# Kernel tuning notes

Hardware: AMD Instinct MI355X
Metric: run time of the kernel (lower is better)

The kernel has to match this reference:

```python
import jax, jax.numpy as jnp
import numpy as np

SEQ_LEN, BATCH, HIDDEN, OUT = 512, 4096, 2048, 10


def setup_inputs() -> dict:
    key = jax.random.key(0)
    ks = jax.random.split(key, 7)
    return {
        "x": jax.random.normal(ks[0], (SEQ_LEN, BATCH), jnp.float32),
        "Wx": jax.random.normal(ks[1], (HIDDEN, 1), jnp.float32) * 0.05,
        "bx": jax.random.normal(ks[2], (HIDDEN,), jnp.float32) * 0.05,
        "Wh": jax.random.normal(ks[3], (1, HIDDEN), jnp.float32) * 0.05,
        "bh": jax.random.normal(ks[4], (1,), jnp.float32) * 0.05,
        "Wy": jax.random.normal(ks[5], (OUT, HIDDEN), jnp.float32) * 0.05,
        "by": jax.random.normal(ks[6], (OUT,), jnp.float32) * 0.05,
    }


def reference(x, Wx, bx, Wh, bh, Wy, by):
    # x: [T, B]; input_dim == 1 structurally (torch code reshapes x[i] to (B, 1)).
    B = x.shape[1]
    H = Wx.shape[0]
    wx = Wx[:, 0]  # [H]

    def step(h, xt):
        # linear_x(x_t): (B,1) @ (1,H) -> outer product, [B, H]
        x_out = xt[:, None] * wx[None, :] + bx
        # linear_h(h): [B, H] @ [H, 1] -> [B, 1], broadcasts into the add (as in torch)
        h_out = h @ Wh.T + bh
        h_new = jnp.tanh(x_out + h_out)
        return h_new, None

    h0 = jnp.zeros((B, H), x.dtype)
    h_final, _ = jax.lax.scan(step, h0, x)
    logits = h_final @ Wy.T + by  # [B, OUT]
    return jax.nn.softmax(logits, axis=-1)
```

## Files before the change

kernel.cpp:

```cpp
#include <hip/hip_runtime.h>
#include <math.h>


#define SEQ   512
#define BATCH 4096
#define HID   2048
#define NOUT  10
#define KPL   32
#define NS    560
#define ROWQ  9

#define S_LOc   (-10.0f)
#define S_H     (20.0f / 559.0f)
#define S_INVH  (559.0f / 20.0f)
#define S_BIAS  (10.0f * S_INVH)
#define NSM1F   559.0f
#define NSM4F   556.0f
#define U_SCALE (8.0f / 14.0f)
#define U_BIAS  4.0f
#define UCMAXF  7.99951f

#define TABLE_FLOATS (NS * ROWQ * 4)
#define WSA_FLOATS (4096 + 14 * 4096)
#define WSB_FLOATS (4096 + 4 * 4096)
#define DZ14 43.0f
#define DZ9  69.875f

__device__ __forceinline__ float fast_exp2(float v) { return __builtin_amdgcn_exp2f(v); }
__device__ __forceinline__ float fast_rcp(float v)  { return __builtin_amdgcn_rcpf(v); }
__device__ __forceinline__ float med3(float a, float lo, float hi) {
    return __builtin_amdgcn_fmed3f(a, lo, hi);
}
__device__ __forceinline__ float fast_tanh(float a) {
    const float C = 2.8853900817779268f;
    return __builtin_fmaf(-2.0f, fast_rcp(fast_exp2(C * a) + 1.0f), 1.0f);
}
__device__ __forceinline__ float wave_sum(float v) {
#pragma unroll
    for (int m = 1; m < 64; m <<= 1) v += __shfl_xor(v, m, 64);
    return v;
}
__device__ __forceinline__ float combine_eval(float z255, int nn, float dz,
                                              const float* baseA, const float* baseB,
                                              int split, int b) {
    float p = z255 / dz;
    int   c = min(max((int)floorf(p) - 1, 0), nn - 4);
    float t = p - (float)c;
    float a0 = t, a1 = t - 1.0f, a2 = t - 2.0f, a3 = t - 3.0f;
    float m01 = a0 * a1, m23 = a2 * a3;
    float w0 = a1 * m23 * (-1.0f / 6.0f), w1 = a0 * m23 * 0.5f;
    float w2 = m01 * a3 * (-0.5f),        w3 = m01 * a2 * (1.0f / 6.0f);
    float y[4];
#pragma unroll
    for (int i = 0; i < 4; ++i) {
        int n = c + i;
        const float* ptr = (n < split) ? (baseA + (size_t)n * 4096)
                                       : (baseB + (size_t)(n - split) * 4096);
        y[i] = ptr[b];
    }
    return __builtin_fmaf(w0, y[0], w1 * y[1]) + __builtin_fmaf(w2, y[2], w3 * y[3]);
}

__global__ __launch_bounds__(256) void k_coef(const float* __restrict__ Wx, const float* __restrict__ bx,
                                              const float* __restrict__ Wh, const float* __restrict__ bh,
                                              float* __restrict__ tab_g) {
    __shared__ float red[256];
    __shared__ float Gn[32];
    const int k    = blockIdx.x;
    const int node = threadIdx.x & 31;
    const int jc   = threadIdx.x >> 5;
    const int cell = node >> 2, nn = node & 3;
    const float sn = S_LOc + (float)k * S_H;
    const float xi_n = (nn == 0) ? 0.923879533f : (nn == 1) ? 0.382683432f
                     : (nn == 2) ? -0.382683432f : -0.923879533f;
    const float un = (-7.0f + ((float)cell + 0.5f) * 1.75f) + 0.875f * xi_n;
    float p = 0.0f;
    const int j0 = jc * 256;
#pragma unroll 4
    for (int j = j0; j < j0 + 256; ++j)
        p += Wh[j] * fast_tanh(__builtin_fmaf(Wx[j], un, bx[j] + sn));
    red[threadIdx.x] = p;
    __syncthreads();
    if (threadIdx.x < 32) {
        float V = bh[0];
#pragma unroll
        for (int c = 0; c < 8; ++c) V += red[threadIdx.x + 32 * c];
        Gn[threadIdx.x] = __builtin_fmaf(V, S_INVH, S_BIAS);
    }
    __syncthreads();
    float4* wq = (float4*)tab_g;
    if (threadIdx.x < 8) {
        const int c = threadIdx.x;
        float G0 = Gn[4*c+0], G1 = Gn[4*c+1], G2 = Gn[4*c+2], G3 = Gn[4*c+3];
        float d03 = G0 - G3, d12 = G1 - G2;
        float a0 = 0.25f * (G0 + G1 + G2 + G3);
        float a1 = 0.5f * (0.923879533f * d03 + 0.382683432f * d12);
        float a2 = 0.5f * 0.707106781f * (G0 - G1 - G2 + G3);
        float a3 = 0.5f * (0.382683432f * d03 - 0.923879533f * d12);
        wq[k * ROWQ + c] = make_float4(a0 - a2, a1 - 3.0f * a3, 2.0f * a2, 4.0f * a3);
    } else if (threadIdx.x == 8) {
        wq[k * ROWQ + 8] = make_float4(0.f, 0.f, 0.f, 0.f);
    }
}

__global__ __launch_bounds__(256) void k_scan_seg(const float* __restrict__ x,
                                                  const float* __restrict__ bh,
                                                  const float* __restrict__ tab_g,
                                                  float* __restrict__ z255,
                                                  float* __restrict__ baseA,
                                                  float* __restrict__ baseB,
                                                  int split, float dz) {
    __shared__ float4 tabs[5200];
    {
        const float4* src = (const float4*)tab_g;
        for (int i = threadIdx.x; i < NS * ROWQ; i += 256) tabs[i] = src[i];
    }
    __syncthreads();
    const int blk = blockIdx.x;
    const int seg  = (blk < 16) ? 0 : 1;
    const int node = seg ? (blk - 16) >> 4 : 0;
    const int eb   = seg ? (blk - 16) & 15 : blk;
    const int b    = eb * 256 + threadIdx.x;

    const int t0     = seg ? 255 : 0;
    const int nsteps = seg ? 256 : 255;

    float zm1 = seg ? __builtin_fmaf((float)node, dz, -1.0f)
                    : med3(__builtin_fmaf(bh[0], S_INVH, S_BIAS), 0.0f, NSM1F) - 1.0f;

    auto step1 = [&](float xi, float xi2, int ci) {
        float kf  = med3(zm1, 0.0f, NSM4F);
        int   kzi = (int)kf;
        int   idx = ((kzi << 3) + kzi) + ci;
        float4 q0 = tabs[idx];
        float4 q1 = tabs[idx + ROWQ];
        float4 q2 = tabs[idx + 2 * ROWQ];
        float4 q3 = tabs[idx + 3 * ROWQ];
        float kzf = (float)kzi;
        float zc2 = med3(zm1, -1.0f, 558.0f);
        float e   = zc2 - kzf;
        float c0 = e + 1.0f, c1 = e, c2 = e - 1.0f, c3 = e - 2.0f;
        float n01 = c0 * c1, n23 = c2 * c3;
        float ws0 = c1 * n23 * (-1.0f / 6.0f), ws1 = c0 * n23 * 0.5f;
        float ws2 = n01 * c3 * (-0.5f),        ws3 = n01 * c2 * (1.0f / 6.0f);
        float l0 = __builtin_fmaf(q0.y, xi, q0.x), h0 = __builtin_fmaf(q0.w, xi, q0.z);
        float l1 = __builtin_fmaf(q1.y, xi, q1.x), h1 = __builtin_fmaf(q1.w, xi, q1.z);
        float l2 = __builtin_fmaf(q2.y, xi, q2.x), h2 = __builtin_fmaf(q2.w, xi, q2.z);
        float l3 = __builtin_fmaf(q3.y, xi, q3.x), h3 = __builtin_fmaf(q3.w, xi, q3.z);
        float r0 = __builtin_fmaf(h0, xi2, l0);
        float r1 = __builtin_fmaf(h1, xi2, l1);
        float r2 = __builtin_fmaf(h2, xi2, l2);
        float r3 = __builtin_fmaf(h3, xi2, l3);
        float A  = __builtin_fmaf(ws0, r0, ws1 * r1);
        float B  = __builtin_fmaf(ws2, r2, __builtin_fmaf(ws3, r3, -1.0f));
        zm1 = A + B;
    };

    float cur[8], nxt[8];
#pragma unroll
    for (int i = 0; i < 8; ++i)
        cur[i] = x[(size_t)min(t0 + i, SEQ - 1) * BATCH + b];

    const int full = nsteps >> 3, tail = nsteps & 7;
    for (int c = 0; c < full; ++c) {
        const int nb = t0 + (c + 1) * 8;
#pragma unroll
        for (int i = 0; i < 8; ++i)
            nxt[i] = x[(size_t)min(nb + i, SEQ - 1) * BATCH + b];
        float xiA[8], xi2A[8]; int ciA[8];
#pragma unroll
        for (int i = 0; i < 8; ++i) {
            float uc = med3(__builtin_fmaf(cur[i], U_SCALE, U_BIAS), 0.0f, UCMAXF);
            int   ci = (int)uc;
            float xi = __builtin_fmaf(2.0f, uc - (float)ci, -1.0f);
            xiA[i] = xi; xi2A[i] = xi * xi; ciA[i] = ci;
        }
#pragma unroll
        for (int i = 0; i < 8; ++i) step1(xiA[i], xi2A[i], ciA[i]);
#pragma unroll
        for (int i = 0; i < 8; ++i) cur[i] = nxt[i];
    }
    for (int i = 0; i < tail; ++i) {
        float uc = med3(__builtin_fmaf(cur[i], U_SCALE, U_BIAS), 0.0f, UCMAXF);
        int   ci = (int)uc;
        float xi = __builtin_fmaf(2.0f, uc - (float)ci, -1.0f);
        step1(xi, xi * xi, ci);
    }

    const float z = zm1 + 1.0f;
    if (seg == 0) z255[b] = z;
    else {
        float* p = (node < split) ? (baseA + (size_t)node * 4096)
                                  : (baseB + (size_t)(node - split) * 4096);
        p[b] = z;
    }
}

__global__ __launch_bounds__(256) void k_combine(const float* __restrict__ baseA,
                                                 const float* __restrict__ baseB,
                                                 int split, int nn, float dz,
                                                 float* __restrict__ zs) {
    const int b = blockIdx.x * 256 + threadIdx.x;
    float zz = combine_eval(zs[b], nn, dz, baseA, baseB, split, b);
    zs[b] = __builtin_fmaf(zz, S_H, S_LOc);
}

__global__ __launch_bounds__(256) void head_combine_A(
    const float* __restrict__ x,  const float* __restrict__ Wx,
    const float* __restrict__ bx, const float* __restrict__ Wy,
    const float* __restrict__ by, const float* __restrict__ ws,
    float* __restrict__ out)
{
    const int lane = threadIdx.x & 63;
    const int wave = threadIdx.x >> 6;
    const int b    = blockIdx.x * 4 + wave;

    float zz = combine_eval(ws[b], 14, DZ14, ws + 4096, ws + 4096, 14, b);
    const float s = __builtin_fmaf(zz, S_H, S_LOc);

    const float C  = 2.8853900817779268f;
    const float u  = x[(size_t)(SEQ - 1) * BATCH + b];
    const float sc = s * C;
    float acc[NOUT];
#pragma unroll
    for (int i = 0; i < NOUT; ++i) acc[i] = 0.0f;
#pragma unroll 4
    for (int k = 0; k < KPL; ++k) {
        const int j = k * 64 + lane;
        float arg = __builtin_fmaf(u, Wx[j] * C, bx[j] * C) + sc;
        float r   = fast_rcp(fast_exp2(arg) + 1.0f);
        float th  = __builtin_fmaf(-2.0f, r, 1.0f);
#pragma unroll
        for (int i = 0; i < NOUT; ++i)
            acc[i] = __builtin_fmaf(Wy[i * HID + j], th, acc[i]);
    }
#pragma unroll
    for (int i = 0; i < NOUT; ++i) acc[i] = wave_sum(acc[i]) + by[i];
    float m = acc[0];
#pragma unroll
    for (int i = 1; i < NOUT; ++i) m = fmaxf(m, acc[i]);
    const float L2E = 1.4426950408889634f;
    float ev[NOUT]; float Z = 0.0f;
#pragma unroll
    for (int i = 0; i < NOUT; ++i) { ev[i] = fast_exp2((acc[i] - m) * L2E); Z += ev[i]; }
    const float rz = fast_rcp(Z);
    if (lane == 0) {
#pragma unroll
        for (int i = 0; i < NOUT; ++i) out[(size_t)b * NOUT + i] = ev[i] * rz;
    }
}

__global__ __launch_bounds__(256) void rnn_scan_exact(
    const float* __restrict__ x,  const float* __restrict__ Wx,
    const float* __restrict__ bx, const float* __restrict__ Wh,
    const float* __restrict__ bh, float* __restrict__ s_out)
{
    const int lane = threadIdx.x & 63;
    const int wave = threadIdx.x >> 6;
    const int b    = blockIdx.x * 4 + wave;
    const float C = 2.8853900817779268f;
    float wxs[KPL], bxs[KPL], whn[KPL];
    float swh = 0.0f;
#pragma unroll
    for (int k = 0; k < KPL; ++k) {
        const int j = k * 64 + lane;
        const float w = Wh[j];
        wxs[k] = Wx[j] * C; bxs[k] = bx[j] * C; whn[k] = -2.0f * w; swh += w;
    }
    swh = wave_sum(swh);
    const float bh0 = bh[0];
    const float K0  = bh0 + swh;
    float s = bh0, u = x[b];
    for (int t = 0; t < SEQ - 1; ++t) {
        float u_next = x[(size_t)(t + 1) * BATCH + b];
        const float sc = s * C;
        float p = 0.0f;
#pragma unroll
        for (int k = 0; k < KPL; ++k) {
            float arg = __builtin_fmaf(u, wxs[k], bxs[k]) + sc;
            float r   = fast_rcp(fast_exp2(arg) + 1.0f);
            p = __builtin_fmaf(whn[k], r, p);
        }
        s = K0 + wave_sum(p);
        u = u_next;
    }
    if (lane == 0) s_out[b] = s;
}

__global__ __launch_bounds__(256) void rnn_head_exact(
    const float* __restrict__ x,  const float* __restrict__ Wx,
    const float* __restrict__ bx, const float* __restrict__ Wy,
    const float* __restrict__ by, const float* __restrict__ s_in,
    float* __restrict__ out)
{
    const int lane = threadIdx.x & 63;
    const int wave = threadIdx.x >> 6;
    const int b    = blockIdx.x * 4 + wave;
    const float C  = 2.8853900817779268f;
    const float s  = s_in[b];
    const float u  = x[(size_t)(SEQ - 1) * BATCH + b];
    const float sc = s * C;
    float acc[NOUT];
#pragma unroll
    for (int i = 0; i < NOUT; ++i) acc[i] = 0.0f;
#pragma unroll 4
    for (int k = 0; k < KPL; ++k) {
        const int j = k * 64 + lane;
        float arg = __builtin_fmaf(u, Wx[j] * C, bx[j] * C) + sc;
        float r   = fast_rcp(fast_exp2(arg) + 1.0f);
        float th  = __builtin_fmaf(-2.0f, r, 1.0f);
#pragma unroll
        for (int i = 0; i < NOUT; ++i)
            acc[i] = __builtin_fmaf(Wy[i * HID + j], th, acc[i]);
    }
#pragma unroll
    for (int i = 0; i < NOUT; ++i) acc[i] = wave_sum(acc[i]) + by[i];
    float m = acc[0];
#pragma unroll
    for (int i = 1; i < NOUT; ++i) m = fmaxf(m, acc[i]);
    const float L2E = 1.4426950408889634f;
    float ev[NOUT]; float Z = 0.0f;
#pragma unroll
    for (int i = 0; i < NOUT; ++i) { ev[i] = fast_exp2((acc[i] - m) * L2E); Z += ev[i]; }
    const float rz = fast_rcp(Z);
    if (lane == 0) {
#pragma unroll
        for (int i = 0; i < NOUT; ++i) out[(size_t)b * NOUT + i] = ev[i] * rz;
    }
}

extern "C" void kernel_launch(void* const* d_in, const int* in_sizes, int n_in,
                              void* d_out, int out_size, void* d_ws, size_t ws_size,
                              hipStream_t stream)
{
    const float* x  = (const float*)d_in[0];
    const float* Wx = (const float*)d_in[1];
    const float* bx = (const float*)d_in[2];
    const float* Wh = (const float*)d_in[3];
    const float* bh = (const float*)d_in[4];
    const float* Wy = (const float*)d_in[5];
    const float* by = (const float*)d_in[6];
    float* out = (float*)d_out;
    float* wf  = (float*)d_ws;

    if (ws_size >= (size_t)WSA_FLOATS * sizeof(float)) {
        k_coef<<<NS, 256, 0, stream>>>(Wx, bx, Wh, bh, out);
        k_scan_seg<<<16 + 14 * 16, 256, 0, stream>>>(x, bh, out, wf,
                                                     wf + 4096, wf + 4096, 14, DZ14);
        head_combine_A<<<BATCH / 4, 256, 0, stream>>>(x, Wx, bx, Wy, by, wf, out);
    } else if (ws_size >= (size_t)WSB_FLOATS * sizeof(float)) {
        k_coef<<<NS, 256, 0, stream>>>(Wx, bx, Wh, bh, out);
        k_scan_seg<<<16 + 9 * 16, 256, 0, stream>>>(x, bh, out, wf,
                                                    out + TABLE_FLOATS, wf + 4096, 5, DZ9);
        k_combine<<<16, 256, 0, stream>>>(out + TABLE_FLOATS, wf + 4096, 5, 9, DZ9, wf);
        rnn_head_exact<<<BATCH / 4, 256, 0, stream>>>(x, Wx, bx, Wy, by, wf, out);
    } else {
        rnn_scan_exact<<<BATCH / 4, 256, 0, stream>>>(x, Wx, bx, Wh, bh, wf);
        rnn_head_exact<<<BATCH / 4, 256, 0, stream>>>(x, Wx, bx, Wy, by, wf, out);
    }
}
```

Measured before the change: 141.0 us.

## Speculate table index with linear interpolation to shorten serial scan dependency chain

The per-step table lookup in the sequential scan now takes its row index from a cheaply computed linear-interpolation estimate (zf), while the accurate cubic-Lagrange value (za) is computed alongside and resynchronized every 8 steps. The aim is to take the LDS load latency and cubic weight computation off the loop-carried critical path. Index arithmetic also moves to byte offsets with the -1 bias folded into the table pointer. The risk is that wrong rows get selected when the linear estimate drifts from the cubic one, which changes numerical results.

```diff
diff --git a/kernel.cpp b/kernel.cpp
--- a/kernel.cpp
+++ b/kernel.cpp
@@ -15,7 +15,6 @@
 #define S_INVH  (559.0f / 20.0f)
 #define S_BIAS  (10.0f * S_INVH)
 #define NSM1F   559.0f
-#define NSM4F   556.0f
 #define U_SCALE (8.0f / 14.0f)
 #define U_BIAS  4.0f
 #define UCMAXF  7.99951f
@@ -116,6 +115,7 @@
         for (int i = threadIdx.x; i < NS * ROWQ; i += 256) tabs[i] = src[i];
     }
     __syncthreads();
+    const char* tabc = (const char*)tabs;
     const int blk = blockIdx.x;
     const int seg  = (blk < 16) ? 0 : 1;
     const int node = seg ? (blk - 16) >> 4 : 0;
@@ -125,20 +125,47 @@
     const int t0     = seg ? 255 : 0;
     const int nsteps = seg ? 256 : 255;
 
-    float zm1 = seg ? __builtin_fmaf((float)node, dz, -1.0f)
-                    : med3(__builtin_fmaf(bh[0], S_INVH, S_BIAS), 0.0f, NSM1F) - 1.0f;
-
-    auto step1 = [&](float xi, float xi2, int ci) {
-        float kf  = med3(zm1, 0.0f, NSM4F);
-        int   kzi = (int)kf;
-        int   idx = ((kzi << 3) + kzi) + ci;
-        float4 q0 = tabs[idx];
-        float4 q1 = tabs[idx + ROWQ];
-        float4 q2 = tabs[idx + 2 * ROWQ];
-        float4 q3 = tabs[idx + 3 * ROWQ];
-        float kzf = (float)kzi;
-        float zc2 = med3(zm1, -1.0f, 558.0f);
-        float e   = zc2 - kzf;
+    float za = seg ? (float)node * dz
+                   : med3(__builtin_fmaf(bh[0], S_INVH, S_BIAS), 0.0f, NSM1F);
+    float zf = za;
+
+    auto stepF = [&](float xi, float xi2, int cib) {
+        float m  = med3(zf, 1.0f, 557.0f);
+        int   km = (int)m;
+        const float4* qp = (const float4*)(tabc + (km * 144 + cib));
+        float4 q1 = qp[ROWQ];
+        float4 q2 = qp[2 * ROWQ];
+        float4 q0 = qp[0];
+        float4 q3 = qp[3 * ROWQ];
+        float kmf = (float)km;
+        float tf  = zf - kmf;
+        float e   = med3(za, 0.0f, NSM1F) - kmf;
+        float c0 = e + 1.0f, c1 = e, c2 = e - 1.0f, c3 = e - 2.0f;
+        float n01 = c0 * c1, n23 = c2 * c3;
+        float ws0 = c1 * n23 * (-1.0f / 6.0f), ws1 = c0 * n23 * 0.5f;
+        float ws2 = n01 * c3 * (-0.5f),        ws3 = n01 * c2 * (1.0f / 6.0f);
+        float l1 = __builtin_fmaf(q1.y, xi, q1.x), h1 = __builtin_fmaf(q1.w, xi, q1.z);
+        float l2 = __builtin_fmaf(q2.y, xi, q2.x), h2 = __builtin_fmaf(q2.w, xi, q2.z);
+        float r1 = __builtin_fmaf(h1, xi2, l1);
+        float r2 = __builtin_fmaf(h2, xi2, l2);
+        zf = __builtin_fmaf(tf, r2 - r1, r1);
+        float l0 = __builtin_fmaf(q0.y, xi, q0.x), h0 = __builtin_fmaf(q0.w, xi, q0.z);
+        float l3 = __builtin_fmaf(q3.y, xi, q3.x), h3 = __builtin_fmaf(q3.w, xi, q3.z);
+        float r0 = __builtin_fmaf(h0, xi2, l0);
+        float r3 = __builtin_fmaf(h3, xi2, l3);
+        za = __builtin_fmaf(ws0, r0, ws1 * r1) + __builtin_fmaf(ws2, r2, ws3 * r3);
+    };
+
+    auto stepA = [&](float xi, float xi2, int cib) {
+        float m  = med3(za, 1.0f, 557.0f);
+        int   km = (int)m;
+        const float4* qp = (const float4*)(tabc + (km * 144 + cib));
+        float4 q0 = qp[0];
+        float4 q1 = qp[ROWQ];
+        float4 q2 = qp[2 * ROWQ];
+        float4 q3 = qp[3 * ROWQ];
+        float kmf = (float)km;
+        float e   = med3(za, 0.0f, NSM1F) - kmf;
         float c0 = e + 1.0f, c1 = e, c2 = e - 1.0f, c3 = e - 2.0f;
         float n01 = c0 * c1, n23 = c2 * c3;
         float ws0 = c1 * n23 * (-1.0f / 6.0f), ws1 = c0 * n23 * 0.5f;
@@ -151,9 +178,7 @@
         float r1 = __builtin_fmaf(h1, xi2, l1);
         float r2 = __builtin_fmaf(h2, xi2, l2);
         float r3 = __builtin_fmaf(h3, xi2, l3);
-        float A  = __builtin_fmaf(ws0, r0, ws1 * r1);
-        float B  = __builtin_fmaf(ws2, r2, __builtin_fmaf(ws3, r3, -1.0f));
-        zm1 = A + B;
+        za = __builtin_fmaf(ws0, r0, ws1 * r1) + __builtin_fmaf(ws2, r2, ws3 * r3);
     };
 
     float cur[8], nxt[8];
@@ -167,16 +192,17 @@
 #pragma unroll
         for (int i = 0; i < 8; ++i)
             nxt[i] = x[(size_t)min(nb + i, SEQ - 1) * BATCH + b];
-        float xiA[8], xi2A[8]; int ciA[8];
+        float xiA[8], xi2A[8]; int cibA[8];
 #pragma unroll
         for (int i = 0; i < 8; ++i) {
             float uc = med3(__builtin_fmaf(cur[i], U_SCALE, U_BIAS), 0.0f, UCMAXF);
             int   ci = (int)uc;
             float xi = __builtin_fmaf(2.0f, uc - (float)ci, -1.0f);
-            xiA[i] = xi; xi2A[i] = xi * xi; ciA[i] = ci;
+            xiA[i] = xi; xi2A[i] = xi * xi; cibA[i] = (ci << 4) - 144;
         }
 #pragma unroll
-        for (int i = 0; i < 8; ++i) step1(xiA[i], xi2A[i], ciA[i]);
+        for (int i = 0; i < 8; ++i) stepF(xiA[i], xi2A[i], cibA[i]);
+        zf = za;
 #pragma unroll
         for (int i = 0; i < 8; ++i) cur[i] = nxt[i];
     }
@@ -184,10 +210,10 @@
         float uc = med3(__builtin_fmaf(cur[i], U_SCALE, U_BIAS), 0.0f, UCMAXF);
         int   ci = (int)uc;
         float xi = __builtin_fmaf(2.0f, uc - (float)ci, -1.0f);
-        step1(xi, xi * xi, ci);
-    }
-
-    const float z = zm1 + 1.0f;
+        stepA(xi, xi * xi, (ci << 4) - 144);
+    }
+
+    const float z = za;
     if (seg == 0) z255[b] = z;
     else {
         float* p = (node < split) ? (baseA + (size_t)node * 4096)
```

Result: no change. 141.7 us (+0.6%).

## Split scan step into fast linear predictor and deferred cubic correction with manual LDS pipelining

Applied to the files above, without the earlier changes.

Restructures the serial recurrence step so that the critical path only depends on a cheap linear interpolation between the two middle table rows (zf). The full cubic Lagrange evaluation (za) is computed one step later, overlapped with the next step's LDS reads. Hand-written ds_read_b128 with explicit waitcnts and sched barriers control the latency hiding. This shortens the per-step dependency chain, but the index now comes from an approximate z, which risks accuracy drift. It also depends on inline asm and a raw LDS address cast.

```diff
diff --git a/kernel.cpp b/kernel.cpp
--- a/kernel.cpp
+++ b/kernel.cpp
@@ -15,7 +15,6 @@
 #define S_INVH  (559.0f / 20.0f)
 #define S_BIAS  (10.0f * S_INVH)
 #define NSM1F   559.0f
-#define NSM4F   556.0f
 #define U_SCALE (8.0f / 14.0f)
 #define U_BIAS  4.0f
 #define UCMAXF  7.99951f
@@ -25,6 +24,8 @@
 #define WSB_FLOATS (4096 + 4 * 4096)
 #define DZ14 43.0f
 #define DZ9  69.875f
+
+typedef float f32x4 __attribute__((ext_vector_type(4)));
 
 __device__ __forceinline__ float fast_exp2(float v) { return __builtin_amdgcn_exp2f(v); }
 __device__ __forceinline__ float fast_rcp(float v)  { return __builtin_amdgcn_rcpf(v); }
@@ -103,6 +104,51 @@
     }
 }
 
+
+#define STEP_BODY(xi_, xi2_, cib_, FIRST)                                      \
+{                                                                              \
+    float m_   = med3(zf, 1.0f, 557.0f);                                       \
+    int   km_  = (int)m_;                                                      \
+    float kmf_ = (float)km_;                                                   \
+    float tf_  = med3(zf - kmf_, -1.0f, 2.0f);                                 \
+    int   ab_  = km_ * 144 + (cib_);                                           \
+    f32x4 q0_, q1_, q2_, q3_;                                                  \
+    asm volatile("ds_read_b128 %0, %4 offset:144\n\t"                          \
+                 "ds_read_b128 %1, %4 offset:288\n\t"                          \
+                 "ds_read_b128 %2, %4 offset:0\n\t"                            \
+                 "ds_read_b128 %3, %4 offset:432"                              \
+                 : "=v"(q1_), "=v"(q2_), "=v"(q0_), "=v"(q3_)                  \
+                 : "v"(ab_) : "memory");                                       \
+    if (!(FIRST)) {                                                            \
+        asm volatile("s_waitcnt lgkmcnt(4)" ::: "memory");                     \
+        __builtin_amdgcn_sched_barrier(0);                                     \
+        float e_  = med3(za, 0.0f, NSM1F) - kmfp;                              \
+        float c0_ = e_ + 1.0f, c1_ = e_, c2_ = e_ - 1.0f, c3_ = e_ - 2.0f;     \
+        float n01_ = c0_ * c1_, n23_ = c2_ * c3_;                              \
+        float w0_ = c1_ * n23_ * (-1.0f / 6.0f), w1_ = c0_ * n23_ * 0.5f;      \
+        float w2_ = n01_ * c3_ * (-0.5f),        w3_ = n01_ * c2_ * (1.0f/6.0f);\
+        float l0_ = __builtin_fmaf(p0[1], xip, p0[0]);                         \
+        float h0_ = __builtin_fmaf(p0[3], xip, p0[2]);                         \
+        float l3_ = __builtin_fmaf(p3[1], xip, p3[0]);                         \
+        float h3_ = __builtin_fmaf(p3[3], xip, p3[2]);                         \
+        float r0_ = __builtin_fmaf(h0_, xi2p, l0_);                            \
+        float r3_ = __builtin_fmaf(h3_, xi2p, l3_);                            \
+        za = __builtin_fmaf(w0_, r0_, w1_ * r1p)                               \
+           + __builtin_fmaf(w2_, r2p, w3_ * r3_);                              \
+    }                                                                          \
+    asm volatile("s_waitcnt lgkmcnt(2)" ::: "memory");                         \
+    __builtin_amdgcn_sched_barrier(0);                                         \
+    float l1_ = __builtin_fmaf(q1_[1], (xi_), q1_[0]);                         \
+    float h1_ = __builtin_fmaf(q1_[3], (xi_), q1_[2]);                         \
+    float l2_ = __builtin_fmaf(q2_[1], (xi_), q2_[0]);                         \
+    float h2_ = __builtin_fmaf(q2_[3], (xi_), q2_[2]);                         \
+    float r1_ = __builtin_fmaf(h1_, (xi2_), l1_);                              \
+    float r2_ = __builtin_fmaf(h2_, (xi2_), l2_);                              \
+    zf = __builtin_fmaf(tf_, r2_ - r1_, r1_);                                  \
+    p0 = q0_; p3 = q3_;                                                        \
+    xip = (xi_); xi2p = (xi2_); kmfp = kmf_; r1p = r1_; r2p = r2_;             \
+}
+
 __global__ __launch_bounds__(256) void k_scan_seg(const float* __restrict__ x,
                                                   const float* __restrict__ bh,
                                                   const float* __restrict__ tab_g,
@@ -116,6 +162,7 @@
         for (int i = threadIdx.x; i < NS * ROWQ; i += 256) tabs[i] = src[i];
     }
     __syncthreads();
+    const int tb = (int)(size_t)(&tabs[0]);
     const int blk = blockIdx.x;
     const int seg  = (blk < 16) ? 0 : 1;
     const int node = seg ? (blk - 16) >> 4 : 0;
@@ -125,36 +172,12 @@
     const int t0     = seg ? 255 : 0;
     const int nsteps = seg ? 256 : 255;
 
-    float zm1 = seg ? __builtin_fmaf((float)node, dz, -1.0f)
-                    : med3(__builtin_fmaf(bh[0], S_INVH, S_BIAS), 0.0f, NSM1F) - 1.0f;
-
-    auto step1 = [&](float xi, float xi2, int ci) {
-        float kf  = med3(zm1, 0.0f, NSM4F);
-        int   kzi = (int)kf;
-        int   idx = ((kzi << 3) + kzi) + ci;
-        float4 q0 = tabs[idx];
-        float4 q1 = tabs[idx + ROWQ];
-        float4 q2 = tabs[idx + 2 * ROWQ];
-        float4 q3 = tabs[idx + 3 * ROWQ];
-        float kzf = (float)kzi;
-        float zc2 = med3(zm1, -1.0f, 558.0f);
-        float e   = zc2 - kzf;
-        float c0 = e + 1.0f, c1 = e, c2 = e - 1.0f, c3 = e - 2.0f;
-        float n01 = c0 * c1, n23 = c2 * c3;
-        float ws0 = c1 * n23 * (-1.0f / 6.0f), ws1 = c0 * n23 * 0.5f;
-        float ws2 = n01 * c3 * (-0.5f),        ws3 = n01 * c2 * (1.0f / 6.0f);
-        float l0 = __builtin_fmaf(q0.y, xi, q0.x), h0 = __builtin_fmaf(q0.w, xi, q0.z);
-        float l1 = __builtin_fmaf(q1.y, xi, q1.x), h1 = __builtin_fmaf(q1.w, xi, q1.z);
-        float l2 = __builtin_fmaf(q2.y, xi, q2.x), h2 = __builtin_fmaf(q2.w, xi, q2.z);
-        float l3 = __builtin_fmaf(q3.y, xi, q3.x), h3 = __builtin_fmaf(q3.w, xi, q3.z);
-        float r0 = __builtin_fmaf(h0, xi2, l0);
-        float r1 = __builtin_fmaf(h1, xi2, l1);
-        float r2 = __builtin_fmaf(h2, xi2, l2);
-        float r3 = __builtin_fmaf(h3, xi2, l3);
-        float A  = __builtin_fmaf(ws0, r0, ws1 * r1);
-        float B  = __builtin_fmaf(ws2, r2, __builtin_fmaf(ws3, r3, -1.0f));
-        zm1 = A + B;
-    };
+    float za = seg ? (float)node * dz
+                   : med3(__builtin_fmaf(bh[0], S_INVH, S_BIAS), 0.0f, NSM1F);
+    float zf = za;
+
+    f32x4 p0, p3;
+    float xip = 0.0f, xi2p = 0.0f, kmfp = 0.0f, r1p = 0.0f, r2p = 0.0f;
 
     float cur[8], nxt[8];
 #pragma unroll
@@ -162,21 +185,39 @@
         cur[i] = x[(size_t)min(t0 + i, SEQ - 1) * BATCH + b];
 
     const int full = nsteps >> 3, tail = nsteps & 7;
-    for (int c = 0; c < full; ++c) {
-        const int nb = t0 + (c + 1) * 8;
+
+    float xiA[8], xi2A[8]; int cibA[8];
+    {
 #pragma unroll
         for (int i = 0; i < 8; ++i)
-            nxt[i] = x[(size_t)min(nb + i, SEQ - 1) * BATCH + b];
-        float xiA[8], xi2A[8]; int ciA[8];
+            nxt[i] = x[(size_t)min(t0 + 8 + i, SEQ - 1) * BATCH + b];
 #pragma unroll
         for (int i = 0; i < 8; ++i) {
             float uc = med3(__builtin_fmaf(cur[i], U_SCALE, U_BIAS), 0.0f, UCMAXF);
             int   ci = (int)uc;
             float xi = __builtin_fmaf(2.0f, uc - (float)ci, -1.0f);
-            xiA[i] = xi; xi2A[i] = xi * xi; ciA[i] = ci;
+            xiA[i] = xi; xi2A[i] = xi * xi; cibA[i] = tb + (ci << 4) - 144;
         }
-#pragma unroll
-        for (int i = 0; i < 8; ++i) step1(xiA[i], xi2A[i], ciA[i]);
+        STEP_BODY(xiA[0], xi2A[0], cibA[0], 1);
+#pragma unroll
+        for (int i = 1; i < 8; ++i) STEP_BODY(xiA[i], xi2A[i], cibA[i], 0);
+#pragma unroll
+        for (int i = 0; i < 8; ++i) cur[i] = nxt[i];
+    }
+    for (int c = 1; c < full; ++c) {
+        const int nb = t0 + (c + 1) * 8;
+#pragma unroll
+        for (int i = 0; i < 8; ++i)
+            nxt[i] = x[(size_t)min(nb + i, SEQ - 1) * BATCH + b];
+#pragma unroll
+        for (int i = 0; i < 8; ++i) {
+            float uc = med3(__builtin_fmaf(cur[i], U_SCALE, U_BIAS), 0.0f, UCMAXF);
+            int   ci = (int)uc;
+            float xi = __builtin_fmaf(2.0f, uc - (float)ci, -1.0f);
+            xiA[i] = xi; xi2A[i] = xi * xi; cibA[i] = tb + (ci << 4) - 144;
+        }
+#pragma unroll
+        for (int i = 0; i < 8; ++i) STEP_BODY(xiA[i], xi2A[i], cibA[i], 0);
 #pragma unroll
         for (int i = 0; i < 8; ++i) cur[i] = nxt[i];
     }
@@ -184,10 +225,28 @@
         float uc = med3(__builtin_fmaf(cur[i], U_SCALE, U_BIAS), 0.0f, UCMAXF);
         int   ci = (int)uc;
         float xi = __builtin_fmaf(2.0f, uc - (float)ci, -1.0f);
-        step1(xi, xi * xi, ci);
-    }
-
-    const float z = zm1 + 1.0f;
+        float x2 = xi * xi;
+        int  cib = tb + (ci << 4) - 144;
+        STEP_BODY(xi, x2, cib, 0);
+    }
+    asm volatile("s_waitcnt lgkmcnt(0)" ::: "memory");
+    __builtin_amdgcn_sched_barrier(0);
+    {
+        float e  = med3(za, 0.0f, NSM1F) - kmfp;
+        float c0 = e + 1.0f, c1 = e, c2 = e - 1.0f, c3 = e - 2.0f;
+        float n01 = c0 * c1, n23 = c2 * c3;
+        float w0 = c1 * n23 * (-1.0f / 6.0f), w1 = c0 * n23 * 0.5f;
+        float w2 = n01 * c3 * (-0.5f),        w3 = n01 * c2 * (1.0f / 6.0f);
+        float l0 = __builtin_fmaf(p0[1], xip, p0[0]);
+        float h0 = __builtin_fmaf(p0[3], xip, p0[2]);
+        float l3 = __builtin_fmaf(p3[1], xip, p3[0]);
+        float h3 = __builtin_fmaf(p3[3], xip, p3[2]);
+        float r0 = __builtin_fmaf(h0, xi2p, l0);
+        float r3 = __builtin_fmaf(h3, xi2p, l3);
+        za = __builtin_fmaf(w0, r0, w1 * r1p) + __builtin_fmaf(w2, r2p, w3 * r3);
+    }
+
+    const float z = za;
     if (seg == 0) z255[b] = z;
     else {
         float* p = (node < split) ? (baseA + (size_t)node * 4096)
```

New measurement: 141.3 us. About the same (+0.2%).
